# Performance work log

Hardware: AMD Instinct MI355X
Metric: run time of the kernel (lower is better)

## Reference

```python
import jax, jax.numpy as jnp
import numpy as np
import math

N_HEADS = 16
D_EMBED = 1024
D_HEAD = D_EMBED // N_HEADS
SEQ_LEN = 4096
N_GRAPHS = 16


def setup_inputs() -> dict:
    key = jax.random.key(0)
    ks = jax.random.split(key, 6)
    x = jax.random.normal(ks[0], (SEQ_LEN, D_EMBED), dtype=jnp.float32)
    batch = jnp.sort(jax.random.randint(ks[1], (SEQ_LEN,), 0, N_GRAPHS, dtype=jnp.int64))
    s_in = 1.0 / math.sqrt(D_EMBED)
    W_in = jax.random.normal(ks[2], (D_EMBED, 3 * D_EMBED), dtype=jnp.float32) * s_in
    b_in = jnp.zeros((3 * D_EMBED,), dtype=jnp.float32)
    W_out = jax.random.normal(ks[3], (D_EMBED, D_EMBED), dtype=jnp.float32) * s_in
    b_out = jnp.zeros((D_EMBED,), dtype=jnp.float32)
    return {"x": x, "batch": batch, "W_in": W_in, "b_in": b_in, "W_out": W_out, "b_out": b_out}


def reference(x, batch, W_in, b_in, W_out, b_out):
    # x: [N, D]; batch: [N] graph ids
    n, d = x.shape
    qkv = x @ W_in + b_in                      # [N, 3D]
    q, k, v = jnp.split(qkv, 3, axis=-1)
    # [N, H, dh] -> [H, N, dh]
    q = q.reshape(n, N_HEADS, D_HEAD).transpose(1, 0, 2)
    k = k.reshape(n, N_HEADS, D_HEAD).transpose(1, 0, 2)
    v = v.reshape(n, N_HEADS, D_HEAD).transpose(1, 0, 2)
    weight = jnp.einsum('hnd,hmd->hnm', q, k)  # [H, N, N]
    # Faithful to original: in-block mask value is 1.0 (not 0), out-of-block -inf,
    # added BEFORE dividing by sqrt(d_head).
    same = batch[:, None] == batch[None, :]
    mask = jnp.where(same, 1.0, -jnp.inf).astype(weight.dtype)
    weight = (weight + mask) / math.sqrt(D_HEAD)
    weight = jax.nn.softmax(weight, axis=-1)
    out = jnp.einsum('hnm,hmd->hnd', weight, v)  # [H, N, dh]
    out = out.transpose(1, 0, 2).reshape(n, d)
    return out @ W_out + b_out
```

## Files before the change

kernel.cpp:

```cpp
#include <hip/hip_runtime.h>
#include <math.h>

#define NT 4096
#define DE 1024
#define NH 16
#define DH 64
#define NG 16

typedef unsigned short u16;
typedef __attribute__((ext_vector_type(8))) short short8;
typedef __attribute__((ext_vector_type(4))) float f32x4;

__device__ __forceinline__ u16 f2bf(float f) {
    unsigned u = __float_as_uint(f);
    unsigned r = (u + 0x7FFF + ((u >> 16) & 1)) >> 16;
    return (u16)r;
}
__device__ __forceinline__ u16 f2bf_trunc(float f) {
    return (u16)(__float_as_uint(f) >> 16);
}

__device__ __forceinline__ void gld_lds16(const u16* g, u16* l) {
    __builtin_amdgcn_global_load_lds(
        (const __attribute__((address_space(1))) unsigned int*)g,
        (__attribute__((address_space(3))) unsigned int*)l, 16, 0, 0);
}

__global__ __launch_bounds__(256) void cast_bounds_k(
        const float* __restrict__ in, u16* __restrict__ out, int n4,
        const int* __restrict__ batch, int* __restrict__ bounds) {
    if (blockIdx.x == 0 && threadIdx.x <= NG) {
        int g = threadIdx.x;
        int lo = 0, hi = NT;
        while (lo < hi) {
            int mid = (lo + hi) >> 1;
            if (batch[mid] < g) lo = mid + 1;
            else hi = mid;
        }
        bounds[g] = lo;
    }
    int i = blockIdx.x * blockDim.x + threadIdx.x;
    if (i < n4) {
        float4 v = *(const float4*)(in + (size_t)i * 4);
        ushort4 o = make_ushort4(f2bf(v.x), f2bf(v.y), f2bf(v.z), f2bf(v.w));
        *(ushort4*)(out + (size_t)i * 4) = o;
    }
}

__device__ __forceinline__ void transpose_tile(
        const float* __restrict__ W, u16* __restrict__ Wt, int K, int N,
        int k0, int n0, int t) {
    __shared__ float Ls[32][33];
    int row = t >> 3;
    int c4  = (t & 7) * 4;
    float4 v = *(const float4*)(W + (size_t)(k0 + row) * N + n0 + c4);
    Ls[row][c4 + 0] = v.x; Ls[row][c4 + 1] = v.y;
    Ls[row][c4 + 2] = v.z; Ls[row][c4 + 3] = v.w;
    __syncthreads();
    ushort4 o = make_ushort4(f2bf(Ls[c4 + 0][row]), f2bf(Ls[c4 + 1][row]),
                             f2bf(Ls[c4 + 2][row]), f2bf(Ls[c4 + 3][row]));
    *(ushort4*)(Wt + (size_t)(n0 + row) * K + k0 + c4) = o;
}

__global__ __launch_bounds__(256) void transpose_both_k(
        const float* __restrict__ W_in, u16* __restrict__ Wt_in,
        const float* __restrict__ W_out, u16* __restrict__ Wt_out) {
    int kx = blockIdx.x * 32;
    int y  = blockIdx.y;
    if (y < 96)
        transpose_tile(W_in, Wt_in, DE, 3 * DE, kx, y * 32, threadIdx.x);
    else
        transpose_tile(W_out, Wt_out, DE, DE, kx, (y - 96) * 32, threadIdx.x);
}

template<typename OutT>
__global__ __launch_bounds__(256) void gemm_mfma_bt(
        const u16* __restrict__ A, const u16* __restrict__ Bt,
        const float* __restrict__ bias, OutT* __restrict__ C,
        int M, int N, int K) {
    __shared__ u16 As[128 * 32];
    __shared__ u16 Bs[128 * 32];
    const int tid  = threadIdx.x;
    const int wave = tid >> 6;
    const int lane = tid & 63;
    const int l15  = lane & 15;
    const int quad = lane >> 4;
    const int m0 = blockIdx.y * 128;
    const int n0 = blockIdx.x * 128;
    const int wm = (wave >> 1) * 64;
    const int wn = (wave & 1) * 64;

    f32x4 acc[4][4];
#pragma unroll
    for (int i = 0; i < 4; ++i)
#pragma unroll
        for (int j = 0; j < 4; ++j) acc[i][j] = (f32x4){0.f, 0.f, 0.f, 0.f};

    const int srow = lane >> 2;
    const int scol = (lane & 3) * 8;

    for (int k0 = 0; k0 < K; k0 += 32) {
#pragma unroll
        for (int i = 0; i < 2; ++i) {
            int c   = wave * 2 + i;
            int row = c * 16 + srow;
            gld_lds16(A  + (size_t)(m0 + row) * K + k0 + scol, &As[c * 512]);
            gld_lds16(Bt + (size_t)(n0 + row) * K + k0 + scol, &Bs[c * 512]);
        }
        __syncthreads();

        short8 af[4], bf[4];
#pragma unroll
        for (int it = 0; it < 4; ++it)
            af[it] = *(const short8*)&As[(wm + 16 * it + l15) * 32 + quad * 8];
#pragma unroll
        for (int jt = 0; jt < 4; ++jt)
            bf[jt] = *(const short8*)&Bs[(wn + 16 * jt + l15) * 32 + quad * 8];
#pragma unroll
        for (int it = 0; it < 4; ++it)
#pragma unroll
            for (int jt = 0; jt < 4; ++jt)
                acc[it][jt] = __builtin_amdgcn_mfma_f32_16x16x32_bf16(
                    af[it], bf[jt], acc[it][jt], 0, 0, 0);
        __syncthreads();
    }

#pragma unroll
    for (int jt = 0; jt < 4; ++jt) {
        int col = n0 + wn + 16 * jt + l15;
        float bv = bias[col];
#pragma unroll
        for (int it = 0; it < 4; ++it) {
            int rbase = m0 + wm + 16 * it + quad * 4;
#pragma unroll
            for (int r = 0; r < 4; ++r) {
                float v = acc[it][jt][r] + bv;
                if constexpr (sizeof(OutT) == 2)
                    C[(size_t)(rbase + r) * N + col] = (OutT)f2bf(v);
                else
                    C[(size_t)(rbase + r) * N + col] = v;
            }
        }
    }
}

__global__ __launch_bounds__(256) void attn_mfma_k(
        const u16* __restrict__ qkv, const int* __restrict__ bounds,
        u16* __restrict__ out) {
    const int h  = blockIdx.x;
    const int g  = blockIdx.y;
    const int qt = blockIdx.z;
    const int s0 = bounds[g];
    const int s1 = bounds[g + 1];
    const int q0 = s0 + qt * 64;
    if (q0 >= s1) return;
    const int nq = min(64, s1 - q0);

    __shared__ u16 Ks[64][72];
    __shared__ u16 Vt[64][72];
    __shared__ u16 Ps[64][72];

    const int tid  = threadIdx.x;
    const int wave = tid >> 6;
    const int lane = tid & 63;
    const int l15  = lane & 15;
    const int quad = lane >> 4;

    short8 qf[2];
    {
        int qrow = wave * 16 + l15;
        uint4 a = {0, 0, 0, 0}, b = {0, 0, 0, 0};
        if (qrow < nq) {
            const u16* src = qkv + (size_t)(q0 + qrow) * 3072 + h * 64 + quad * 8;
            a = *(const uint4*)src;
            b = *(const uint4*)(src + 32);
        }
        qf[0] = *(short8*)&a;
        qf[1] = *(short8*)&b;
    }

    short8 onesf;
#pragma unroll
    for (int j = 0; j < 8; ++j) onesf[j] = (short)0x3F80;

    f32x4 o_acc[4];
    f32x4 l_acc = (f32x4){0.f, 0.f, 0.f, 0.f};
#pragma unroll
    for (int ct = 0; ct < 4; ++ct) o_acc[ct] = (f32x4){0.f, 0.f, 0.f, 0.f};

    for (int k0 = s0; k0 < s1; k0 += 64) {
        const int nk = min(64, s1 - k0);
        __syncthreads();

        {
            int row = tid >> 2;
            int c0  = (tid & 3) * 16;
            uint4 a = {0, 0, 0, 0}, b = {0, 0, 0, 0};
            if (row < nk) {
                const u16* src = qkv + (size_t)(k0 + row) * 3072 + 1024 + h * 64 + c0;
                a = *(const uint4*)src;
                b = *(const uint4*)(src + 8);
            }
            *(uint4*)&Ks[row][c0]     = a;
            *(uint4*)&Ks[row][c0 + 8] = b;
        }
        {
            int rp = tid & 31;
            int c0 = (tid >> 5) * 8;
            int r0 = 2 * rp, r1 = 2 * rp + 1;
            uint4 a = {0, 0, 0, 0}, b = {0, 0, 0, 0};
            if (r0 < nk) a = *(const uint4*)(qkv + (size_t)(k0 + r0) * 3072 + 2048 + h * 64 + c0);
            if (r1 < nk) b = *(const uint4*)(qkv + (size_t)(k0 + r1) * 3072 + 2048 + h * 64 + c0);
            const u16* pa = (const u16*)&a;
            const u16* pb = (const u16*)&b;
#pragma unroll
            for (int j = 0; j < 8; ++j) {
                unsigned w = (unsigned)pa[j] | ((unsigned)pb[j] << 16);
                *(unsigned*)&Vt[c0 + j][r0] = w;
            }
        }
        __syncthreads();

        f32x4 s[4];
#pragma unroll
        for (int ct = 0; ct < 4; ++ct) {
            short8 kf0 = *(const short8*)&Ks[ct * 16 + l15][quad * 8];
            short8 kf1 = *(const short8*)&Ks[ct * 16 + l15][quad * 8 + 32];
            f32x4 acc = (f32x4){0.f, 0.f, 0.f, 0.f};
            acc = __builtin_amdgcn_mfma_f32_16x16x32_bf16(qf[0], kf0, acc, 0, 0, 0);
            acc = __builtin_amdgcn_mfma_f32_16x16x32_bf16(qf[1], kf1, acc, 0, 0, 0);
            s[ct] = acc;
        }

#pragma unroll
        for (int ct = 0; ct < 4; ++ct) {
            bool valid = (k0 + ct * 16 + l15) < s1;
#pragma unroll
            for (int r = 0; r < 4; ++r) {
                float pv = valid ? __expf(s[ct][r] * 0.125f) : 0.f;
                Ps[wave * 16 + quad * 4 + r][ct * 16 + l15] = f2bf_trunc(pv);
            }
        }

        short8 pf0 = *(const short8*)&Ps[wave * 16 + l15][quad * 8];
        short8 pf1 = *(const short8*)&Ps[wave * 16 + l15][quad * 8 + 32];

        l_acc = __builtin_amdgcn_mfma_f32_16x16x32_bf16(pf0, onesf, l_acc, 0, 0, 0);
        l_acc = __builtin_amdgcn_mfma_f32_16x16x32_bf16(pf1, onesf, l_acc, 0, 0, 0);

#pragma unroll
        for (int ct = 0; ct < 4; ++ct) {
            short8 vf0 = *(const short8*)&Vt[ct * 16 + l15][quad * 8];
            short8 vf1 = *(const short8*)&Vt[ct * 16 + l15][quad * 8 + 32];
            o_acc[ct] = __builtin_amdgcn_mfma_f32_16x16x32_bf16(pf0, vf0, o_acc[ct], 0, 0, 0);
            o_acc[ct] = __builtin_amdgcn_mfma_f32_16x16x32_bf16(pf1, vf1, o_acc[ct], 0, 0, 0);
        }
    }

#pragma unroll
    for (int r = 0; r < 4; ++r) {
        int row = wave * 16 + quad * 4 + r;
        if (row < nq) {
            float inv = 1.f / l_acc[r];
#pragma unroll
            for (int ct = 0; ct < 4; ++ct)
                out[(size_t)(q0 + row) * 1024 + h * 64 + ct * 16 + l15] =
                    f2bf(o_acc[ct][r] * inv);
        }
    }
}

extern "C" void kernel_launch(void* const* d_in, const int* in_sizes, int n_in,
                              void* d_out, int out_size, void* d_ws, size_t ws_size,
                              hipStream_t stream) {
    const float* x     = (const float*)d_in[0];
    const int*   batch = (const int*)d_in[1];
    const float* W_in  = (const float*)d_in[2];
    const float* b_in  = (const float*)d_in[3];
    const float* W_out = (const float*)d_in[4];
    const float* b_out = (const float*)d_in[5];
    float* out = (float*)d_out;

    u16* qkvb   = (u16*)d_ws;
    u16* attnb  = qkvb + (size_t)NT * 3 * DE;
    u16* xb     = attnb + (size_t)NT * DE;
    u16* Wt_in  = xb + (size_t)NT * DE;
    u16* Wt_out = Wt_in + (size_t)3 * DE * DE;
    int* bounds = (int*)(Wt_out + (size_t)DE * DE);

    cast_bounds_k<<<NT * DE / 4 / 256, 256, 0, stream>>>(
        x, xb, NT * DE / 4, batch, bounds);
    transpose_both_k<<<dim3(DE / 32, 128), 256, 0, stream>>>(
        W_in, Wt_in, W_out, Wt_out);

    gemm_mfma_bt<u16><<<dim3(3 * DE / 128, NT / 128), 256, 0, stream>>>(
        xb, Wt_in, b_in, qkvb, NT, 3 * DE, DE);

    attn_mfma_k<<<dim3(NH, NG, NT / 64), 256, 0, stream>>>(qkvb, bounds, attnb);

    gemm_mfma_bt<float><<<dim3(DE / 128, NT / 128), 256, 0, stream>>>(
        attnb, Wt_out, b_out, out, NT, DE, DE);
}
```

Baseline: 170.6 us.

## Fuse prep kernels, widen GEMM K-tile with XOR-swizzled LDS, retile output GEMM

Merges the cast/bounds kernel and the weight transpose kernel into one prep launch. The GEMM now loads a 64-wide K slice per iteration into an XOR-swizzled LDS layout, which halves the number of barriers and is meant to avoid bank conflicts. The tile shape becomes a template, and the output projection uses 64x128 tiles so more blocks fill the GPU. In exchange it uses more LDS per block and adds swizzle index arithmetic.

```diff
diff --git a/kernel.cpp b/kernel.cpp
--- a/kernel.cpp
+++ b/kernel.cpp
@@ -26,31 +26,34 @@
         (__attribute__((address_space(3))) unsigned int*)l, 16, 0, 0);
 }
 
-__global__ __launch_bounds__(256) void cast_bounds_k(
-        const float* __restrict__ in, u16* __restrict__ out, int n4,
-        const int* __restrict__ batch, int* __restrict__ bounds) {
-    if (blockIdx.x == 0 && threadIdx.x <= NG) {
-        int g = threadIdx.x;
-        int lo = 0, hi = NT;
-        while (lo < hi) {
-            int mid = (lo + hi) >> 1;
-            if (batch[mid] < g) lo = mid + 1;
-            else hi = mid;
-        }
-        bounds[g] = lo;
-    }
-    int i = blockIdx.x * blockDim.x + threadIdx.x;
-    if (i < n4) {
-        float4 v = *(const float4*)(in + (size_t)i * 4);
+__global__ __launch_bounds__(256) void prep_k(
+        const float* __restrict__ x, u16* __restrict__ xb,
+        const int* __restrict__ batch, int* __restrict__ bounds,
+        const float* __restrict__ W_in, u16* __restrict__ Wt_in,
+        const float* __restrict__ W_out, u16* __restrict__ Wt_out) {
+    __shared__ float Ls[32][33];
+    int bid = blockIdx.x;
+    int t = threadIdx.x;
+    if (bid < 4096) {
+        if (bid == 0 && t <= NG) {
+            int g = t, lo = 0, hi = NT;
+            while (lo < hi) {
+                int mid = (lo + hi) >> 1;
+                if (batch[mid] < g) lo = mid + 1;
+                else hi = mid;
+            }
+            bounds[g] = lo;
+        }
+        int i = bid * 256 + t;
+        float4 v = *(const float4*)(x + (size_t)i * 4);
         ushort4 o = make_ushort4(f2bf(v.x), f2bf(v.y), f2bf(v.z), f2bf(v.w));
-        *(ushort4*)(out + (size_t)i * 4) = o;
-    }
-}
-
-__device__ __forceinline__ void transpose_tile(
-        const float* __restrict__ W, u16* __restrict__ Wt, int K, int N,
-        int k0, int n0, int t) {
-    __shared__ float Ls[32][33];
+        *(ushort4*)(xb + (size_t)i * 4) = o;
+        return;
+    }
+    int tb = bid - 4096;
+    const float* W; u16* Wt; int N, k0, n0;
+    if (tb < 3072) { W = W_in;  Wt = Wt_in;  N = 3 * DE; k0 = (tb & 31) * 32; n0 = (tb >> 5) * 32; }
+    else { tb -= 3072; W = W_out; Wt = Wt_out; N = DE;   k0 = (tb & 31) * 32; n0 = (tb >> 5) * 32; }
     int row = t >> 3;
     int c4  = (t & 7) * 4;
     float4 v = *(const float4*)(W + (size_t)(k0 + row) * N + n0 + c4);
@@ -59,78 +62,71 @@
     __syncthreads();
     ushort4 o = make_ushort4(f2bf(Ls[c4 + 0][row]), f2bf(Ls[c4 + 1][row]),
                              f2bf(Ls[c4 + 2][row]), f2bf(Ls[c4 + 3][row]));
-    *(ushort4*)(Wt + (size_t)(n0 + row) * K + k0 + c4) = o;
-}
-
-__global__ __launch_bounds__(256) void transpose_both_k(
-        const float* __restrict__ W_in, u16* __restrict__ Wt_in,
-        const float* __restrict__ W_out, u16* __restrict__ Wt_out) {
-    int kx = blockIdx.x * 32;
-    int y  = blockIdx.y;
-    if (y < 96)
-        transpose_tile(W_in, Wt_in, DE, 3 * DE, kx, y * 32, threadIdx.x);
-    else
-        transpose_tile(W_out, Wt_out, DE, DE, kx, (y - 96) * 32, threadIdx.x);
-}
-
-template<typename OutT>
+    *(ushort4*)(Wt + (size_t)(n0 + row) * DE + k0 + c4) = o;
+}
+
+template<int FM, int FN, typename OutT>
 __global__ __launch_bounds__(256) void gemm_mfma_bt(
         const u16* __restrict__ A, const u16* __restrict__ Bt,
         const float* __restrict__ bias, OutT* __restrict__ C,
         int M, int N, int K) {
-    __shared__ u16 As[128 * 32];
-    __shared__ u16 Bs[128 * 32];
+    __shared__ u16 As[32 * FM * 64];
+    __shared__ u16 Bs[32 * FN * 64];
     const int tid  = threadIdx.x;
     const int wave = tid >> 6;
     const int lane = tid & 63;
     const int l15  = lane & 15;
     const int quad = lane >> 4;
-    const int m0 = blockIdx.y * 128;
-    const int n0 = blockIdx.x * 128;
-    const int wm = (wave >> 1) * 64;
-    const int wn = (wave & 1) * 64;
-
-    f32x4 acc[4][4];
-#pragma unroll
-    for (int i = 0; i < 4; ++i)
-#pragma unroll
-        for (int j = 0; j < 4; ++j) acc[i][j] = (f32x4){0.f, 0.f, 0.f, 0.f};
-
-    const int srow = lane >> 2;
-    const int scol = (lane & 3) * 8;
-
-    for (int k0 = 0; k0 < K; k0 += 32) {
-#pragma unroll
-        for (int i = 0; i < 2; ++i) {
-            int c   = wave * 2 + i;
-            int row = c * 16 + srow;
-            gld_lds16(A  + (size_t)(m0 + row) * K + k0 + scol, &As[c * 512]);
-            gld_lds16(Bt + (size_t)(n0 + row) * K + k0 + scol, &Bs[c * 512]);
-        }
-        __syncthreads();
-
-        short8 af[4], bf[4];
-#pragma unroll
-        for (int it = 0; it < 4; ++it)
-            af[it] = *(const short8*)&As[(wm + 16 * it + l15) * 32 + quad * 8];
-#pragma unroll
-        for (int jt = 0; jt < 4; ++jt)
-            bf[jt] = *(const short8*)&Bs[(wn + 16 * jt + l15) * 32 + quad * 8];
-#pragma unroll
-        for (int it = 0; it < 4; ++it)
-#pragma unroll
-            for (int jt = 0; jt < 4; ++jt)
-                acc[it][jt] = __builtin_amdgcn_mfma_f32_16x16x32_bf16(
-                    af[it], bf[jt], acc[it][jt], 0, 0, 0);
-        __syncthreads();
-    }
-
-#pragma unroll
-    for (int jt = 0; jt < 4; ++jt) {
+    const int m0 = blockIdx.y * 32 * FM;
+    const int n0 = blockIdx.x * 32 * FN;
+    const int wm = (wave >> 1) * 16 * FM;
+    const int wn = (wave & 1) * 16 * FN;
+
+    f32x4 acc[FM][FN];
+#pragma unroll
+    for (int i = 0; i < FM; ++i)
+#pragma unroll
+        for (int j = 0; j < FN; ++j) acc[i][j] = (f32x4){0.f, 0.f, 0.f, 0.f};
+
+    const int srow = lane >> 3;
+    const int scol = ((lane & 7) ^ srow) * 8;
+    const int xq   = l15 & 7;
+
+    for (int k0 = 0; k0 < K; k0 += 64) {
+#pragma unroll
+        for (int s = wave; s < 4 * FM; s += 4)
+            gld_lds16(A + (size_t)(m0 + s * 8 + srow) * K + k0 + scol, &As[s * 512]);
+#pragma unroll
+        for (int s = wave; s < 4 * FN; s += 4)
+            gld_lds16(Bt + (size_t)(n0 + s * 8 + srow) * K + k0 + scol, &Bs[s * 512]);
+        __syncthreads();
+
+#pragma unroll
+        for (int kh = 0; kh < 2; ++kh) {
+            const int xb_ = 4 * kh + quad;
+            short8 af[FM], bf[FN];
+#pragma unroll
+            for (int it = 0; it < FM; ++it)
+                af[it] = *(const short8*)&As[(wm + 16 * it + l15) * 64 + ((xb_ ^ xq) * 8)];
+#pragma unroll
+            for (int jt = 0; jt < FN; ++jt)
+                bf[jt] = *(const short8*)&Bs[(wn + 16 * jt + l15) * 64 + ((xb_ ^ xq) * 8)];
+#pragma unroll
+            for (int it = 0; it < FM; ++it)
+#pragma unroll
+                for (int jt = 0; jt < FN; ++jt)
+                    acc[it][jt] = __builtin_amdgcn_mfma_f32_16x16x32_bf16(
+                        af[it], bf[jt], acc[it][jt], 0, 0, 0);
+        }
+        __syncthreads();
+    }
+
+#pragma unroll
+    for (int jt = 0; jt < FN; ++jt) {
         int col = n0 + wn + 16 * jt + l15;
         float bv = bias[col];
 #pragma unroll
-        for (int it = 0; it < 4; ++it) {
+        for (int it = 0; it < FM; ++it) {
             int rbase = m0 + wm + 16 * it + quad * 4;
 #pragma unroll
             for (int r = 0; r < 4; ++r) {
@@ -288,16 +284,13 @@
     u16* Wt_out = Wt_in + (size_t)3 * DE * DE;
     int* bounds = (int*)(Wt_out + (size_t)DE * DE);
 
-    cast_bounds_k<<<NT * DE / 4 / 256, 256, 0, stream>>>(
-        x, xb, NT * DE / 4, batch, bounds);
-    transpose_both_k<<<dim3(DE / 32, 128), 256, 0, stream>>>(
-        W_in, Wt_in, W_out, Wt_out);
-
-    gemm_mfma_bt<u16><<<dim3(3 * DE / 128, NT / 128), 256, 0, stream>>>(
+    prep_k<<<8192, 256, 0, stream>>>(x, xb, batch, bounds, W_in, Wt_in, W_out, Wt_out);
+
+    gemm_mfma_bt<4, 4, u16><<<dim3(3 * DE / 128, NT / 128), 256, 0, stream>>>(
         xb, Wt_in, b_in, qkvb, NT, 3 * DE, DE);
 
     attn_mfma_k<<<dim3(NH, NG, NT / 64), 256, 0, stream>>>(qkvb, bounds, attnb);
 
-    gemm_mfma_bt<float><<<dim3(DE / 128, NT / 128), 256, 0, stream>>>(
+    gemm_mfma_bt<2, 4, float><<<dim3(DE / 128, NT / 64), 256, 0, stream>>>(
         attnb, Wt_out, b_out, out, NT, DE, DE);
 }
```

New measurement: 161.2 us. 1.06x faster.
